# Kernel optimization log

Measured on AMD Instinct MI355X. Metric: run time of the kernel, lower is better.

The kernel has to match this reference:

```python
import jax, jax.numpy as jnp
import numpy as np

B, S, D, H = 2, 2048, 1024, 16
DH = D // H
EPS = 1e-12


def setup_inputs() -> dict:
    key = jax.random.key(0)
    ks = jax.random.split(key, 8)
    return {
        "query": jax.random.normal(ks[0], (B, S, D), jnp.float32),
        "key": jax.random.normal(ks[1], (B, S, D), jnp.float32),
        "value": jax.random.normal(ks[2], (B, S, D), jnp.float32),
        "mask": jax.random.randint(ks[3], (B, S), 0, 2, jnp.int32),
        "Wq": jax.random.normal(ks[4], (D, D), jnp.float32) * 0.02,
        "bq": jnp.zeros((D,), jnp.float32),
        "Wk": jax.random.normal(ks[5], (D, D), jnp.float32) * 0.02,
        "bk": jnp.zeros((D,), jnp.float32),
        "Wv": jax.random.normal(ks[6], (D, D), jnp.float32) * 0.02,
        "bv": jnp.zeros((D,), jnp.float32),
        "gamma": jnp.ones((D,), jnp.float32),
        "beta": jnp.zeros((D,), jnp.float32),
    }


def _split_heads(x):
    # [B,S,D] -> [B,H,S,DH]
    return x.reshape(B, S, H, DH).transpose(0, 2, 1, 3)


def reference(query, key, value, mask, Wq, bq, Wk, bk, Wv, bv, gamma, beta):
    q = _split_heads(query @ Wq + bq)
    k = _split_heads(key @ Wk + bk)
    v = _split_heads(value @ Wv + bv)

    scale = 1.0 / jnp.sqrt(jnp.float32(DH))
    scores = jnp.einsum("bhqd,bhkd->bhqk", q, k) * scale  # [B,H,S,S]
    maskf = mask.astype(jnp.float32)  # [B,S]
    scores = scores - 10000.0 * (1.0 - maskf[:, None, None, :])
    attn = jax.nn.softmax(scores, axis=-1)  # dropout disabled (eval mode)

    h = jnp.einsum("bhqk,bhkd->bhqd", attn, v)
    h = h.transpose(0, 2, 1, 3).reshape(B, S, D)

    x = query + h
    u = jnp.mean(x, axis=-1, keepdims=True)
    s = jnp.mean((x - u) ** 2, axis=-1, keepdims=True)
    xn = (x - u) / jnp.sqrt(s + EPS)
    return gamma * xn + beta
```

## Files before the change

### kernel.cpp

```cpp
#include <hip/hip_runtime.h>
#include <math.h>

#define B_  2
#define S_  2048
#define D_  1024
#define H_  16
#define DH_ 64
#define M_  (B_*S_)

typedef short v8s  __attribute__((ext_vector_type(8)));
typedef float v4f  __attribute__((ext_vector_type(4)));
typedef float f32x16 __attribute__((ext_vector_type(16)));
typedef unsigned short u16;

__device__ __forceinline__ u16 f2bf(float f) {
    unsigned u = __float_as_uint(f);
    u = u + 0x7FFFu + ((u >> 16) & 1u);
    return (u16)(u >> 16);
}
__device__ __forceinline__ u16 f2bf_t(float f) {
    return (u16)(__float_as_uint(f) >> 16);
}

__global__ __launch_bounds__(256)
void cvt_bf16_kernel(const float* __restrict__ X0, const float* __restrict__ X1,
                     const float* __restrict__ X2, u16* __restrict__ Y)
{
    const float* X = (blockIdx.y == 0) ? X0 : (blockIdx.y == 1) ? X1 : X2;
    u16* out = Y + (size_t)blockIdx.y * M_ * D_;
    const size_t i = ((size_t)blockIdx.x * 256 + threadIdx.x) * 8;
    float4 a = *(const float4*)&X[i];
    float4 b = *(const float4*)&X[i + 4];
    u16 tmp[8];
    tmp[0] = f2bf(a.x); tmp[1] = f2bf(a.y); tmp[2] = f2bf(a.z); tmp[3] = f2bf(a.w);
    tmp[4] = f2bf(b.x); tmp[5] = f2bf(b.y); tmp[6] = f2bf(b.z); tmp[7] = f2bf(b.w);
    *(v8s*)&out[i] = *(v8s*)&tmp[0];
}

__global__ __launch_bounds__(256)
void transpose_w_kernel(const float* __restrict__ W0, const float* __restrict__ W1,
                        const float* __restrict__ W2, u16* __restrict__ WtAll)
{
    __shared__ u16 TS[64][66];
    const float* W = (blockIdx.z == 0) ? W0 : (blockIdx.z == 1) ? W1 : W2;
    u16* out = WtAll + (size_t)blockIdx.z * D_ * D_;
    const int k0 = blockIdx.x * 64;
    const int n0 = blockIdx.y * 64;
    const int t = threadIdx.x;
    const int r = t >> 2, c = t & 3;

    #pragma unroll
    for (int u = 0; u < 4; ++u) {
        int nc = (c + 4 * u) * 4;
        float4 v = *(const float4*)&W[(size_t)(k0 + r) * D_ + n0 + nc];
        TS[r][nc + 0] = f2bf(v.x); TS[r][nc + 1] = f2bf(v.y);
        TS[r][nc + 2] = f2bf(v.z); TS[r][nc + 3] = f2bf(v.w);
    }
    __syncthreads();
    u16 tmp[16];
    #pragma unroll
    for (int u = 0; u < 16; ++u) tmp[u] = TS[c * 16 + u][r];
    u16* dst = &out[(size_t)(n0 + r) * D_ + k0 + c * 16];
    *(v8s*)&dst[0] = *(v8s*)&tmp[0];
    *(v8s*)&dst[8] = *(v8s*)&tmp[8];
}

__global__ __launch_bounds__(256)
void qkv_gemm_kernel(const u16* __restrict__ XbfAll, const u16* __restrict__ WtAll,
                     const float* __restrict__ bq, const float* __restrict__ bk2,
                     const float* __restrict__ bv2,
                     u16* __restrict__ Qh, u16* __restrict__ Kh, u16* __restrict__ Vt)
{
    __shared__ u16 SA[128 * 64];
    __shared__ u16 SB[128 * 64];

    const int z = blockIdx.z;
    const u16* X  = XbfAll + (size_t)z * M_ * D_;
    const u16* Wt = WtAll  + (size_t)z * D_ * D_;
    const float* bias = (z == 0) ? bq : (z == 1) ? bk2 : bv2;

    const int t = threadIdx.x;
    const int lane = t & 63;
    const int w = t >> 6;
    const int l31 = lane & 31;
    const int half = lane >> 5;
    const int wr = (w >> 1) * 64;
    const int wc = (w & 1) * 64;
    const int row0 = blockIdx.y * 128;
    const int col0 = blockIdx.x * 128;

    f32x16 acc[2][2];
    #pragma unroll
    for (int mb = 0; mb < 2; ++mb)
        #pragma unroll
        for (int nb = 0; nb < 2; ++nb)
            acc[mb][nb] = (f32x16)(0.0f);

    const int srow = t >> 3;
    const int pch  = t & 7;

    for (int k0 = 0; k0 < D_; k0 += 64) {
        __syncthreads();
        #pragma unroll
        for (int c = 0; c < 4; ++c) {
            const int r = c * 32 + srow;
            const int lch = pch ^ (r & 7);
            const u16* asrc = &X [(size_t)(row0 + r) * D_ + k0 + lch * 8];
            const u16* bsrc = &Wt[(size_t)(col0 + r) * D_ + k0 + lch * 8];
            __builtin_amdgcn_global_load_lds(
                (const __attribute__((address_space(1))) void*)asrc,
                (__attribute__((address_space(3))) void*)&SA[r * 64 + pch * 8],
                16, 0, 0);
            __builtin_amdgcn_global_load_lds(
                (const __attribute__((address_space(1))) void*)bsrc,
                (__attribute__((address_space(3))) void*)&SB[r * 64 + pch * 8],
                16, 0, 0);
        }
        __syncthreads();

        #pragma unroll
        for (int ks = 0; ks < 4; ++ks) {
            v8s av[2], bv[2];
            #pragma unroll
            for (int mb = 0; mb < 2; ++mb) {
                const int r = wr + mb * 32 + l31;
                const int ch = (ks * 2 + half) ^ (r & 7);
                av[mb] = *(const v8s*)&SA[r * 64 + ch * 8];
            }
            #pragma unroll
            for (int nb = 0; nb < 2; ++nb) {
                const int r = wc + nb * 32 + l31;
                const int ch = (ks * 2 + half) ^ (r & 7);
                bv[nb] = *(const v8s*)&SB[r * 64 + ch * 8];
            }
            #pragma unroll
            for (int mb = 0; mb < 2; ++mb)
                #pragma unroll
                for (int nb = 0; nb < 2; ++nb)
                    acc[mb][nb] = __builtin_amdgcn_mfma_f32_32x32x16_bf16(
                        av[mb], bv[nb], acc[mb][nb], 0, 0, 0);
        }
    }

    #pragma unroll
    for (int nb = 0; nb < 2; ++nb) {
        const int col = col0 + wc + nb * 32 + l31;
        const float bb = bias[col];
        const int h = col >> 6, d = col & 63;
        #pragma unroll
        for (int mb = 0; mb < 2; ++mb) {
            #pragma unroll
            for (int rg = 0; rg < 16; ++rg) {
                const int row = row0 + wr + mb * 32 + (rg & 3) + 8 * (rg >> 2) + 4 * half;
                const int b = row >> 11, s = row & (S_ - 1);
                const u16 o = f2bf(acc[mb][nb][rg] + bb);
                if (z == 0)
                    Qh[(((size_t)(b * H_ + h)) * S_ + s) * DH_ + d] = o;
                else if (z == 1)
                    Kh[(((size_t)(b * H_ + h)) * S_ + s) * DH_ + d] = o;
                else
                    Vt[(((size_t)(b * H_ + h)) * DH_ + d) * S_ + s] = o;
            }
        }
    }
}

__global__ __launch_bounds__(256)
void attn_kernel(const u16* __restrict__ Qh, const u16* __restrict__ Kh,
                 const u16* __restrict__ Vt, const int* __restrict__ mask,
                 float* __restrict__ Hout)
{
    __shared__ u16 Ks[64][64];
    __shared__ u16 Vs[64][64];
    __shared__ u16 Ps[4][16][64];
    __shared__ float mb[64];

    const int t = threadIdx.x;
    const int lane = t & 63;
    const int w = t >> 6;
    const int g = lane >> 4;
    const int l15 = lane & 15;
    const int bh = blockIdx.y;
    const int b = bh >> 4;
    const int h = bh & 15;
    const int q0 = blockIdx.x * 64;

    const float SC = 0.18033688011112042f;
    const float MBIAS = -14426.950408889634f;

    v8s aq[2];
    {
        const u16* qb = Qh + ((size_t)bh * S_ + q0 + w * 16 + l15) * DH_;
        aq[0] = *(const v8s*)&qb[g * 8];
        aq[1] = *(const v8s*)&qb[32 + g * 8];
    }

    float lsum[4] = {0.f, 0.f, 0.f, 0.f};
    v4f Of[4];
    #pragma unroll
    for (int j = 0; j < 4; ++j) Of[j] = (v4f){0.f, 0.f, 0.f, 0.f};

    const int sk = t >> 3;
    const int sj = t & 7;
    const int swz_s = (sj ^ (sk & 7)) * 8;

    for (int kt = 0; kt < S_ / 64; ++kt) {
        const int kbase = kt * 64;
        const u16* ksrc0 = Kh + ((size_t)bh * S_ + kbase + sk) * DH_ + sj * 8;
        const u16* ksrc1 = Kh + ((size_t)bh * S_ + kbase + sk + 32) * DH_ + sj * 8;
        v8s kr0 = *(const v8s*)ksrc0;
        v8s kr1 = *(const v8s*)ksrc1;
        const u16* vsrc0 = Vt + ((size_t)bh * DH_ + sk) * S_ + kbase + sj * 8;
        const u16* vsrc1 = Vt + ((size_t)bh * DH_ + sk + 32) * S_ + kbase + sj * 8;
        v8s vr0 = *(const v8s*)vsrc0;
        v8s vr1 = *(const v8s*)vsrc1;
        int mv = 0;
        if (t < 64) mv = mask[b * S_ + kbase + t];

        __syncthreads();
        *(v8s*)&Ks[sk][swz_s]      = kr0;
        *(v8s*)&Ks[sk + 32][swz_s] = kr1;
        *(v8s*)&Vs[sk][swz_s]      = vr0;
        *(v8s*)&Vs[sk + 32][swz_s] = vr1;
        if (t < 64) mb[t] = mv ? 0.0f : MBIAS;
        __syncthreads();

        v4f sc4[4];
        #pragma unroll
        for (int j = 0; j < 4; ++j) sc4[j] = (v4f){0.f, 0.f, 0.f, 0.f};
        #pragma unroll
        for (int j = 0; j < 4; ++j) {
            const int kcol = j * 16 + l15;
            const int sx = kcol & 7;
            v8s bk0 = *(const v8s*)&Ks[kcol][((0 * 4 + g) ^ sx) * 8];
            v8s bk1 = *(const v8s*)&Ks[kcol][((1 * 4 + g) ^ sx) * 8];
            sc4[j] = __builtin_amdgcn_mfma_f32_16x16x32_bf16(aq[0], bk0, sc4[j], 0, 0, 0);
            sc4[j] = __builtin_amdgcn_mfma_f32_16x16x32_bf16(aq[1], bk1, sc4[j], 0, 0, 0);
        }
        float mbj[4];
        #pragma unroll
        for (int j = 0; j < 4; ++j) mbj[j] = mb[j * 16 + l15];

        #pragma unroll
        for (int i = 0; i < 4; ++i) {
            float p0 = __builtin_amdgcn_exp2f(fmaf(sc4[0][i], SC, mbj[0]));
            float p1 = __builtin_amdgcn_exp2f(fmaf(sc4[1][i], SC, mbj[1]));
            float p2 = __builtin_amdgcn_exp2f(fmaf(sc4[2][i], SC, mbj[2]));
            float p3 = __builtin_amdgcn_exp2f(fmaf(sc4[3][i], SC, mbj[3]));
            lsum[i] += (p0 + p1) + (p2 + p3);
            const int q = g * 4 + i;
            const int swz = 8 * (q & 7);
            Ps[w][q][(0 * 16 + l15) ^ swz] = f2bf_t(p0);
            Ps[w][q][(1 * 16 + l15) ^ swz] = f2bf_t(p1);
            Ps[w][q][(2 * 16 + l15) ^ swz] = f2bf_t(p2);
            Ps[w][q][(3 * 16 + l15) ^ swz] = f2bf_t(p3);
        }

        const int sq = l15 & 7;
        v8s pa0 = *(const v8s*)&Ps[w][l15][((0 + g) ^ sq) * 8];
        v8s pa1 = *(const v8s*)&Ps[w][l15][((4 + g) ^ sq) * 8];
        #pragma unroll
        for (int j = 0; j < 4; ++j) {
            const int dcol = j * 16 + l15;
            const int sx = dcol & 7;
            v8s bv0 = *(const v8s*)&Vs[dcol][((0 + g) ^ sx) * 8];
            v8s bv1 = *(const v8s*)&Vs[dcol][((4 + g) ^ sx) * 8];
            Of[j] = __builtin_amdgcn_mfma_f32_16x16x32_bf16(pa0, bv0, Of[j], 0, 0, 0);
            Of[j] = __builtin_amdgcn_mfma_f32_16x16x32_bf16(pa1, bv1, Of[j], 0, 0, 0);
        }
    }

    #pragma unroll
    for (int i = 0; i < 4; ++i) {
        lsum[i] += __shfl_xor(lsum[i], 1, 64);
        lsum[i] += __shfl_xor(lsum[i], 2, 64);
        lsum[i] += __shfl_xor(lsum[i], 4, 64);
        lsum[i] += __shfl_xor(lsum[i], 8, 64);
    }
    float inv[4];
    #pragma unroll
    for (int i = 0; i < 4; ++i) inv[i] = 1.0f / lsum[i];
    #pragma unroll
    for (int j = 0; j < 4; ++j) {
        #pragma unroll
        for (int i = 0; i < 4; ++i) {
            int q = q0 + w * 16 + g * 4 + i;
            Hout[((size_t)(b * S_ + q)) * D_ + h * DH_ + j * 16 + l15] = Of[j][i] * inv[i];
        }
    }
}

__global__ __launch_bounds__(256)
void ln_kernel(const float* __restrict__ query, const float* __restrict__ Hout,
               const float* __restrict__ gamma, const float* __restrict__ beta,
               float* __restrict__ out)
{
    __shared__ float ws1[4], ws2[4];
    const int row = blockIdx.x;
    const int tid = threadIdx.x;
    const size_t base = (size_t)row * D_ + tid * 4;

    float4 xq = *(const float4*)&query[base];
    float4 xh = *(const float4*)&Hout[base];
    float x[4] = { xq.x + xh.x, xq.y + xh.y, xq.z + xh.z, xq.w + xh.w };

    float sum = x[0] + x[1] + x[2] + x[3];
    float sq  = x[0]*x[0] + x[1]*x[1] + x[2]*x[2] + x[3]*x[3];
    #pragma unroll
    for (int off = 32; off >= 1; off >>= 1) {
        sum += __shfl_down(sum, off, 64);
        sq  += __shfl_down(sq,  off, 64);
    }
    if ((tid & 63) == 0) { ws1[tid >> 6] = sum; ws2[tid >> 6] = sq; }
    __syncthreads();
    sum = ws1[0] + ws1[1] + ws1[2] + ws1[3];
    sq  = ws2[0] + ws2[1] + ws2[2] + ws2[3];

    const float u    = sum * (1.0f / D_);
    const float var  = sq * (1.0f / D_) - u * u;
    const float rstd = rsqrtf(var + 1e-12f);

    float4 gv = *(const float4*)&gamma[tid * 4];
    float4 bv = *(const float4*)&beta[tid * 4];
    float4 o;
    o.x = gv.x * (x[0] - u) * rstd + bv.x;
    o.y = gv.y * (x[1] - u) * rstd + bv.y;
    o.z = gv.z * (x[2] - u) * rstd + bv.z;
    o.w = gv.w * (x[3] - u) * rstd + bv.w;
    *(float4*)&out[base] = o;
}

extern "C" void kernel_launch(void* const* d_in, const int* in_sizes, int n_in,
                              void* d_out, int out_size, void* d_ws, size_t ws_size,
                              hipStream_t stream)
{
    const float* query = (const float*)d_in[0];
    const float* key   = (const float*)d_in[1];
    const float* value = (const float*)d_in[2];
    const int*   mask  = (const int*)d_in[3];
    const float* Wq    = (const float*)d_in[4];
    const float* bq    = (const float*)d_in[5];
    const float* Wk    = (const float*)d_in[6];
    const float* bk    = (const float*)d_in[7];
    const float* Wv    = (const float*)d_in[8];
    const float* bv    = (const float*)d_in[9];
    const float* gamma = (const float*)d_in[10];
    const float* beta  = (const float*)d_in[11];
    float* out = (float*)d_out;

    char* ws = (char*)d_ws;
    u16* Xbf = (u16*)ws;                      ws += (size_t)3 * M_ * D_ * sizeof(u16);
    u16* Wt  = (u16*)ws;                      ws += (size_t)3 * D_ * D_ * sizeof(u16);
    u16* Qh  = (u16*)ws;                      ws += (size_t)M_ * D_ * sizeof(u16);
    u16* Kh  = (u16*)ws;                      ws += (size_t)M_ * D_ * sizeof(u16);
    u16* Vt  = (u16*)ws;                      ws += (size_t)M_ * D_ * sizeof(u16);
    float* Ho = (float*)ws;

    cvt_bf16_kernel<<<dim3(M_ * D_ / 2048, 3), 256, 0, stream>>>(query, key, value, Xbf);
    transpose_w_kernel<<<dim3(16, 16, 3), 256, 0, stream>>>(Wq, Wk, Wv, Wt);
    qkv_gemm_kernel<<<dim3(D_ / 128, M_ / 128, 3), 256, 0, stream>>>(
        Xbf, Wt, bq, bk, bv, Qh, Kh, Vt);
    attn_kernel<<<dim3(S_ / 64, B_ * H_), 256, 0, stream>>>(Qh, Kh, Vt, mask, Ho);
    ln_kernel<<<M_, 256, 0, stream>>>(query, Ho, gamma, beta, out);
}
```

Before: 245.0 us.

## Rewrite attention with 32x32 MFMA, register-resident P via permlane swap, ballot mask

The attention kernel moves from 16x16x32 to 32x32x16 MFMA tiles, with 32 query rows per wave and 128 per block. Scores are computed transposed (K as the A operand), so the softmax probabilities can be packed to bf16 and rearranged in registers with v_permlane32_swap. This removes the LDS round trip for P. The mask becomes a wave ballot bitmask that zeroes probabilities, replacing the shared mask-bias array. The V transpose is split out of the GEMM epilogue into a separate tiled transpose kernel, so GEMM stores are uniform, at the cost of an extra launch and buffer.

```diff
diff --git a/kernel.cpp b/kernel.cpp
--- a/kernel.cpp
+++ b/kernel.cpp
@@ -12,14 +12,12 @@
 typedef float v4f  __attribute__((ext_vector_type(4)));
 typedef float f32x16 __attribute__((ext_vector_type(16)));
 typedef unsigned short u16;
+typedef unsigned int u32;
 
 __device__ __forceinline__ u16 f2bf(float f) {
-    unsigned u = __float_as_uint(f);
+    u32 u = __float_as_uint(f);
     u = u + 0x7FFFu + ((u >> 16) & 1u);
     return (u16)(u >> 16);
-}
-__device__ __forceinline__ u16 f2bf_t(float f) {
-    return (u16)(__float_as_uint(f) >> 16);
 }
 
 __global__ __launch_bounds__(256)
@@ -69,7 +67,7 @@
 void qkv_gemm_kernel(const u16* __restrict__ XbfAll, const u16* __restrict__ WtAll,
                      const float* __restrict__ bq, const float* __restrict__ bk2,
                      const float* __restrict__ bv2,
-                     u16* __restrict__ Qh, u16* __restrict__ Kh, u16* __restrict__ Vt)
+                     u16* __restrict__ Qh, u16* __restrict__ Kh, u16* __restrict__ Vh)
 {
     __shared__ u16 SA[128 * 64];
     __shared__ u16 SB[128 * 64];
@@ -78,6 +76,7 @@
     const u16* X  = XbfAll + (size_t)z * M_ * D_;
     const u16* Wt = WtAll  + (size_t)z * D_ * D_;
     const float* bias = (z == 0) ? bq : (z == 1) ? bk2 : bv2;
+    u16* Y = (z == 0) ? Qh : (z == 1) ? Kh : Vh;
 
     const int t = threadIdx.x;
     const int lane = t & 63;
@@ -153,16 +152,35 @@
             for (int rg = 0; rg < 16; ++rg) {
                 const int row = row0 + wr + mb * 32 + (rg & 3) + 8 * (rg >> 2) + 4 * half;
                 const int b = row >> 11, s = row & (S_ - 1);
-                const u16 o = f2bf(acc[mb][nb][rg] + bb);
-                if (z == 0)
-                    Qh[(((size_t)(b * H_ + h)) * S_ + s) * DH_ + d] = o;
-                else if (z == 1)
-                    Kh[(((size_t)(b * H_ + h)) * S_ + s) * DH_ + d] = o;
-                else
-                    Vt[(((size_t)(b * H_ + h)) * DH_ + d) * S_ + s] = o;
-            }
-        }
-    }
+                Y[(((size_t)(b * H_ + h)) * S_ + s) * DH_ + d] = f2bf(acc[mb][nb][rg] + bb);
+            }
+        }
+    }
+}
+
+__global__ __launch_bounds__(256)
+void transpose_v_kernel(const u16* __restrict__ Vh, u16* __restrict__ Vt)
+{
+    __shared__ u16 TS[64][66];
+    const int bh = blockIdx.y;
+    const int s0 = blockIdx.x * 64;
+    const int t = threadIdx.x;
+    const int r = t >> 2, c = t & 3;
+
+    {
+        const u16* src = Vh + ((size_t)(bh * S_ + s0 + r)) * DH_ + c * 16;
+        v8s a = *(const v8s*)&src[0];
+        v8s b = *(const v8s*)&src[8];
+        *(v8s*)&TS[r][c * 16]     = a;
+        *(v8s*)&TS[r][c * 16 + 8] = b;
+    }
+    __syncthreads();
+    u16 tmp[16];
+    #pragma unroll
+    for (int u = 0; u < 16; ++u) tmp[u] = TS[c * 16 + u][r];
+    u16* dst = Vt + ((size_t)(bh * DH_ + r)) * S_ + s0 + c * 16;
+    *(v8s*)&dst[0] = *(v8s*)&tmp[0];
+    *(v8s*)&dst[8] = *(v8s*)&tmp[8];
 }
 
 __global__ __launch_bounds__(256)
@@ -172,121 +190,121 @@
 {
     __shared__ u16 Ks[64][64];
     __shared__ u16 Vs[64][64];
-    __shared__ u16 Ps[4][16][64];
-    __shared__ float mb[64];
+    __shared__ float lsq[4][32];
 
     const int t = threadIdx.x;
     const int lane = t & 63;
     const int w = t >> 6;
-    const int g = lane >> 4;
-    const int l15 = lane & 15;
+    const int l31 = lane & 31;
+    const int half = lane >> 5;
     const int bh = blockIdx.y;
     const int b = bh >> 4;
     const int h = bh & 15;
-    const int q0 = blockIdx.x * 64;
-
+    const int q0 = blockIdx.x * 128 + w * 32;
     const float SC = 0.18033688011112042f;
-    const float MBIAS = -14426.950408889634f;
-
-    v8s aq[2];
+
+    v8s qf[4];
     {
-        const u16* qb = Qh + ((size_t)bh * S_ + q0 + w * 16 + l15) * DH_;
-        aq[0] = *(const v8s*)&qb[g * 8];
-        aq[1] = *(const v8s*)&qb[32 + g * 8];
-    }
-
-    float lsum[4] = {0.f, 0.f, 0.f, 0.f};
-    v4f Of[4];
-    #pragma unroll
-    for (int j = 0; j < 4; ++j) Of[j] = (v4f){0.f, 0.f, 0.f, 0.f};
+        const u16* qb = Qh + ((size_t)bh * S_ + q0 + l31) * DH_;
+        #pragma unroll
+        for (int sp = 0; sp < 4; ++sp)
+            qf[sp] = *(const v8s*)&qb[sp * 16 + half * 8];
+    }
+
+    f32x16 O0 = (f32x16)(0.0f), O1 = (f32x16)(0.0f);
+    float lsum = 0.0f;
 
     const int sk = t >> 3;
     const int sj = t & 7;
-    const int swz_s = (sj ^ (sk & 7)) * 8;
+    const int swz = (sj ^ (sk & 7)) * 8;
+    const int rsw = (l31 & 7);
 
     for (int kt = 0; kt < S_ / 64; ++kt) {
         const int kbase = kt * 64;
-        const u16* ksrc0 = Kh + ((size_t)bh * S_ + kbase + sk) * DH_ + sj * 8;
-        const u16* ksrc1 = Kh + ((size_t)bh * S_ + kbase + sk + 32) * DH_ + sj * 8;
-        v8s kr0 = *(const v8s*)ksrc0;
-        v8s kr1 = *(const v8s*)ksrc1;
-        const u16* vsrc0 = Vt + ((size_t)bh * DH_ + sk) * S_ + kbase + sj * 8;
-        const u16* vsrc1 = Vt + ((size_t)bh * DH_ + sk + 32) * S_ + kbase + sj * 8;
-        v8s vr0 = *(const v8s*)vsrc0;
-        v8s vr1 = *(const v8s*)vsrc1;
-        int mv = 0;
-        if (t < 64) mv = mask[b * S_ + kbase + t];
+        v8s kr0 = *(const v8s*)&Kh[((size_t)bh * S_ + kbase + sk) * DH_ + sj * 8];
+        v8s kr1 = *(const v8s*)&Kh[((size_t)bh * S_ + kbase + sk + 32) * DH_ + sj * 8];
+        v8s vr0 = *(const v8s*)&Vt[((size_t)bh * DH_ + sk) * S_ + kbase + sj * 8];
+        v8s vr1 = *(const v8s*)&Vt[((size_t)bh * DH_ + sk + 32) * S_ + kbase + sj * 8];
+        const int mv = mask[b * S_ + kbase + lane];
+        const unsigned long long mword = __ballot(mv != 0);
 
         __syncthreads();
-        *(v8s*)&Ks[sk][swz_s]      = kr0;
-        *(v8s*)&Ks[sk + 32][swz_s] = kr1;
-        *(v8s*)&Vs[sk][swz_s]      = vr0;
-        *(v8s*)&Vs[sk + 32][swz_s] = vr1;
-        if (t < 64) mb[t] = mv ? 0.0f : MBIAS;
+        *(v8s*)&Ks[sk][swz]      = kr0;
+        *(v8s*)&Ks[sk + 32][swz] = kr1;
+        *(v8s*)&Vs[sk][swz]      = vr0;
+        *(v8s*)&Vs[sk + 32][swz] = vr1;
         __syncthreads();
 
-        v4f sc4[4];
-        #pragma unroll
-        for (int j = 0; j < 4; ++j) sc4[j] = (v4f){0.f, 0.f, 0.f, 0.f};
-        #pragma unroll
-        for (int j = 0; j < 4; ++j) {
-            const int kcol = j * 16 + l15;
-            const int sx = kcol & 7;
-            v8s bk0 = *(const v8s*)&Ks[kcol][((0 * 4 + g) ^ sx) * 8];
-            v8s bk1 = *(const v8s*)&Ks[kcol][((1 * 4 + g) ^ sx) * 8];
-            sc4[j] = __builtin_amdgcn_mfma_f32_16x16x32_bf16(aq[0], bk0, sc4[j], 0, 0, 0);
-            sc4[j] = __builtin_amdgcn_mfma_f32_16x16x32_bf16(aq[1], bk1, sc4[j], 0, 0, 0);
-        }
-        float mbj[4];
-        #pragma unroll
-        for (int j = 0; j < 4; ++j) mbj[j] = mb[j * 16 + l15];
-
-        #pragma unroll
-        for (int i = 0; i < 4; ++i) {
-            float p0 = __builtin_amdgcn_exp2f(fmaf(sc4[0][i], SC, mbj[0]));
-            float p1 = __builtin_amdgcn_exp2f(fmaf(sc4[1][i], SC, mbj[1]));
-            float p2 = __builtin_amdgcn_exp2f(fmaf(sc4[2][i], SC, mbj[2]));
-            float p3 = __builtin_amdgcn_exp2f(fmaf(sc4[3][i], SC, mbj[3]));
-            lsum[i] += (p0 + p1) + (p2 + p3);
-            const int q = g * 4 + i;
-            const int swz = 8 * (q & 7);
-            Ps[w][q][(0 * 16 + l15) ^ swz] = f2bf_t(p0);
-            Ps[w][q][(1 * 16 + l15) ^ swz] = f2bf_t(p1);
-            Ps[w][q][(2 * 16 + l15) ^ swz] = f2bf_t(p2);
-            Ps[w][q][(3 * 16 + l15) ^ swz] = f2bf_t(p3);
-        }
-
-        const int sq = l15 & 7;
-        v8s pa0 = *(const v8s*)&Ps[w][l15][((0 + g) ^ sq) * 8];
-        v8s pa1 = *(const v8s*)&Ps[w][l15][((4 + g) ^ sq) * 8];
-        #pragma unroll
-        for (int j = 0; j < 4; ++j) {
-            const int dcol = j * 16 + l15;
-            const int sx = dcol & 7;
-            v8s bv0 = *(const v8s*)&Vs[dcol][((0 + g) ^ sx) * 8];
-            v8s bv1 = *(const v8s*)&Vs[dcol][((4 + g) ^ sx) * 8];
-            Of[j] = __builtin_amdgcn_mfma_f32_16x16x32_bf16(pa0, bv0, Of[j], 0, 0, 0);
-            Of[j] = __builtin_amdgcn_mfma_f32_16x16x32_bf16(pa1, bv1, Of[j], 0, 0, 0);
-        }
-    }
-
-    #pragma unroll
-    for (int i = 0; i < 4; ++i) {
-        lsum[i] += __shfl_xor(lsum[i], 1, 64);
-        lsum[i] += __shfl_xor(lsum[i], 2, 64);
-        lsum[i] += __shfl_xor(lsum[i], 4, 64);
-        lsum[i] += __shfl_xor(lsum[i], 8, 64);
-    }
-    float inv[4];
-    #pragma unroll
-    for (int i = 0; i < 4; ++i) inv[i] = 1.0f / lsum[i];
-    #pragma unroll
-    for (int j = 0; j < 4; ++j) {
-        #pragma unroll
-        for (int i = 0; i < 4; ++i) {
-            int q = q0 + w * 16 + g * 4 + i;
-            Hout[((size_t)(b * S_ + q)) * D_ + h * DH_ + j * 16 + l15] = Of[j][i] * inv[i];
-        }
+        f32x16 st0 = (f32x16)(0.0f), st1 = (f32x16)(0.0f);
+        #pragma unroll
+        for (int sp = 0; sp < 4; ++sp) {
+            const int ch = ((sp * 2 + half) ^ rsw) * 8;
+            v8s k0 = *(const v8s*)&Ks[l31][ch];
+            v8s k1 = *(const v8s*)&Ks[32 + l31][ch];
+            st0 = __builtin_amdgcn_mfma_f32_32x32x16_bf16(k0, qf[sp], st0, 0, 0, 0);
+            st1 = __builtin_amdgcn_mfma_f32_32x32x16_bf16(k1, qf[sp], st1, 0, 0, 0);
+        }
+
+        const u32 vs0 = ((u32)mword) >> (4 * half);
+        const u32 vs1 = ((u32)(mword >> 32)) >> (4 * half);
+        float p0[16], p1[16];
+        #pragma unroll
+        for (int r = 0; r < 16; ++r) {
+            const int sh = (r & 3) + 8 * (r >> 2);
+            float e0 = __builtin_amdgcn_exp2f(st0[r] * SC);
+            float e1 = __builtin_amdgcn_exp2f(st1[r] * SC);
+            p0[r] = ((vs0 >> sh) & 1u) ? e0 : 0.0f;
+            p1[r] = ((vs1 >> sh) & 1u) ? e1 : 0.0f;
+            lsum += p0[r] + p1[r];
+        }
+
+        u32 w0[8], w1[8];
+        #pragma unroll
+        for (int m = 0; m < 8; ++m) {
+            asm("v_cvt_pk_bf16_f32 %0, %1, %2" : "=v"(w0[m]) : "v"(p0[2*m]), "v"(p0[2*m+1]));
+            asm("v_cvt_pk_bf16_f32 %0, %1, %2" : "=v"(w1[m]) : "v"(p1[2*m]), "v"(p1[2*m+1]));
+        }
+        union PU { u32 u[4]; v8s v; };
+        v8s pa[4];
+        #pragma unroll
+        for (int ksp = 0; ksp < 2; ++ksp) {
+            {
+                u32 a  = w0[4*ksp],     bb = w0[4*ksp+2];
+                u32 a2 = w0[4*ksp+1],   b2 = w0[4*ksp+3];
+                asm("v_permlane32_swap_b32 %0, %1" : "+v"(a),  "+v"(bb));
+                asm("v_permlane32_swap_b32 %0, %1" : "+v"(a2), "+v"(b2));
+                PU pu; pu.u[0] = a; pu.u[1] = a2; pu.u[2] = bb; pu.u[3] = b2;
+                pa[ksp] = pu.v;
+            }
+            {
+                u32 a  = w1[4*ksp],     bb = w1[4*ksp+2];
+                u32 a2 = w1[4*ksp+1],   b2 = w1[4*ksp+3];
+                asm("v_permlane32_swap_b32 %0, %1" : "+v"(a),  "+v"(bb));
+                asm("v_permlane32_swap_b32 %0, %1" : "+v"(a2), "+v"(b2));
+                PU pu; pu.u[0] = a; pu.u[1] = a2; pu.u[2] = bb; pu.u[3] = b2;
+                pa[2 + ksp] = pu.v;
+            }
+        }
+
+        #pragma unroll
+        for (int ks = 0; ks < 4; ++ks) {
+            const int ch = ((ks * 2 + half) ^ rsw) * 8;
+            v8s b0 = *(const v8s*)&Vs[l31][ch];
+            v8s b1 = *(const v8s*)&Vs[32 + l31][ch];
+            O0 = __builtin_amdgcn_mfma_f32_32x32x16_bf16(pa[ks], b0, O0, 0, 0, 0);
+            O1 = __builtin_amdgcn_mfma_f32_32x32x16_bf16(pa[ks], b1, O1, 0, 0, 0);
+        }
+    }
+
+    lsum += __shfl_xor(lsum, 32, 64);
+    if (half == 0) lsq[w][l31] = 1.0f / lsum;
+    #pragma unroll
+    for (int r = 0; r < 16; ++r) {
+        const int qrow = (r & 3) + 8 * (r >> 2) + 4 * half;
+        const float iv = lsq[w][qrow];
+        float* dst = &Hout[((size_t)(b * S_ + q0 + qrow)) * D_ + h * DH_];
+        dst[l31]      = O0[r] * iv;
+        dst[32 + l31] = O1[r] * iv;
     }
 }
 
@@ -353,13 +371,15 @@
     u16* Wt  = (u16*)ws;                      ws += (size_t)3 * D_ * D_ * sizeof(u16);
     u16* Qh  = (u16*)ws;                      ws += (size_t)M_ * D_ * sizeof(u16);
     u16* Kh  = (u16*)ws;                      ws += (size_t)M_ * D_ * sizeof(u16);
+    u16* Vh  = (u16*)ws;                      ws += (size_t)M_ * D_ * sizeof(u16);
     u16* Vt  = (u16*)ws;                      ws += (size_t)M_ * D_ * sizeof(u16);
     float* Ho = (float*)ws;
 
     cvt_bf16_kernel<<<dim3(M_ * D_ / 2048, 3), 256, 0, stream>>>(query, key, value, Xbf);
     transpose_w_kernel<<<dim3(16, 16, 3), 256, 0, stream>>>(Wq, Wk, Wv, Wt);
     qkv_gemm_kernel<<<dim3(D_ / 128, M_ / 128, 3), 256, 0, stream>>>(
-        Xbf, Wt, bq, bk, bv, Qh, Kh, Vt);
-    attn_kernel<<<dim3(S_ / 64, B_ * H_), 256, 0, stream>>>(Qh, Kh, Vt, mask, Ho);
+        Xbf, Wt, bq, bk, bv, Qh, Kh, Vh);
+    transpose_v_kernel<<<dim3(S_ / 64, B_ * H_), 256, 0, stream>>>(Vh, Vt);
+    attn_kernel<<<dim3(S_ / 128, B_ * H_), 256, 0, stream>>>(Qh, Kh, Vt, mask, Ho);
     ln_kernel<<<M_, 256, 0, stream>>>(query, Ho, gamma, beta, out);
 }
```

Result: faster. 227.9 us (-7.0%).
